# Kernel tuning notes

Measured on AMD Instinct MI355X. Metric: run time of the kernel, lower is better.

The kernel has to match this reference:

```python
import jax, jax.numpy as jnp
import numpy as np

N = 100000          # nodes (object pairs)
E = 3200000         # edges between pairs
D_IN = 12           # box-pair features
HID = 1024
OUT = 8             # 4+4 logits
C = 10              # z channels after concat (8 logits + ymin_diff + intersection)
R = 2               # relation feature dim
N_LAYERS = 3
LIT = 2 * C + R     # literals per binary clause


def setup_inputs() -> dict:
    key = jax.random.key(0)
    ks = jax.random.split(key, 10)
    features = jax.random.uniform(ks[0], (N, D_IN), dtype=jnp.float32)
    relations = jax.random.normal(ks[1], (E, R), dtype=jnp.float32)
    sx = jax.random.randint(ks[2], (E,), 0, N, dtype=jnp.int64)
    sy = jax.random.randint(ks[3], (E,), 0, N, dtype=jnp.int64)
    # MLP params (Kaiming-ish scale)
    W1 = jax.random.normal(ks[4], (D_IN, HID), dtype=jnp.float32) * (1.0 / np.sqrt(D_IN))
    b1 = jnp.zeros((HID,), dtype=jnp.float32)
    W2 = jax.random.normal(ks[5], (HID, OUT), dtype=jnp.float32) * (1.0 / np.sqrt(HID))
    b2 = jnp.zeros((OUT,), dtype=jnp.float32)
    # one clause weight per KENN relational layer
    clause_w = jax.random.normal(ks[6], (N_LAYERS,), dtype=jnp.float32) * 0.5
    return {"features": features, "relations": relations, "W1": W1, "b1": b1,
            "W2": W2, "b2": b2, "clause_w": clause_w, "sx": sx, "sy": sy}


def _kenn_layer(z, relations, sx, sy, w):
    # gather-boost-scatter: Godel boost residuum (smooth softmax approximation)
    signs = jnp.where(jnp.arange(LIT) % 2 == 0, 1.0, -1.0).astype(z.dtype)
    g = jnp.concatenate([z[sx], z[sy], relations], axis=1)      # [E, LIT]
    delta = (jax.nn.softplus(w) * jax.nn.softmax(signs * g, axis=1)) * signs
    z = z.at[sx].add(delta[:, :C])
    z = z.at[sy].add(delta[:, C:2 * C])
    return z


def reference(features, relations, W1, b1, W2, b2, clause_w, sx, sy):
    # MLP preactivations (dropout is identity at inference)
    h = jax.nn.relu(features @ W1 + b1)           # [N, 1024]
    z = h @ W2 + b2                               # [N, 8]
    ymin_diff = (features[:, 2] - features[:, -2]) * 10.0
    mask = ((features[:, 0] <= features[:, 5]) & (features[:, 1] >= features[:, 4]) &
            (features[:, 2] <= features[:, -1]) & (features[:, 3] >= features[:, -2]))
    intersection = mask.astype(z.dtype) * 10.0 - 5.0
    z = jnp.concatenate([z, ymin_diff[:, None], intersection[:, None]], axis=1)  # [N, 10]
    for l in range(N_LAYERS):
        z = _kenn_layer(z, relations, sx, sy, clause_w[l])
    z = z[:, :-2]                                 # drop the two auxiliary channels
    za, zb = z[:, :4], z[:, 4:]
    return za, jax.nn.softmax(za, axis=1), zb, jax.nn.softmax(zb, axis=1)
```

## Files before the change

kernel.cpp:

```cpp
#include <hip/hip_runtime.h>
#include <math.h>

constexpr int kN    = 100000;
constexpr int kE    = 3200000;
constexpr int kHid  = 1024;
constexpr int kZrow = 12;

constexpr int kCBShift = 10;
constexpr int kCBNodes = 1 << kCBShift;
constexpr int kCB      = (kN + kCBNodes - 1) / kCBNodes;
constexpr int kCBCap   = 68000;
constexpr int kChunkE  = 1024;
constexpr int kChunkEnt= kChunkE * 2;


__global__ __launch_bounds__(256) void mlp_kernel4(
    const float* __restrict__ feat,
    const float* __restrict__ W1,
    const float* __restrict__ b1,
    const float* __restrict__ W2,
    const float* __restrict__ b2,
    float* __restrict__ z)
{
    __shared__ float red[4][8][64];

    int wave = (int)__builtin_amdgcn_readfirstlane(threadIdx.x >> 6);
    int lane = threadIdx.x & 63;
    int n    = blockIdx.x * 64 + lane;
    bool valid = n < kN;
    int nc   = valid ? n : (kN - 1);

    const float4* fr = reinterpret_cast<const float4*>(feat + (size_t)nc * 12);
    float4 f0 = fr[0], f1 = fr[1], f2 = fr[2];
    float f[12] = {f0.x, f0.y, f0.z, f0.w,
                   f1.x, f1.y, f1.z, f1.w,
                   f2.x, f2.y, f2.z, f2.w};

    float acc[8] = {0,0,0,0,0,0,0,0};
    int k0 = wave * (kHid / 4);
    int k1 = k0 + (kHid / 4);

    #pragma unroll 4
    for (int k = k0; k < k1; ++k) {
        float h = b1[k];
        #pragma unroll
        for (int d = 0; d < 12; ++d) h = fmaf(f[d], W1[d * kHid + k], h);
        h = fmaxf(h, 0.0f);
        #pragma unroll
        for (int o = 0; o < 8; ++o) acc[o] = fmaf(h, W2[k * 8 + o], acc[o]);
    }

    #pragma unroll
    for (int o = 0; o < 8; ++o) red[wave][o][lane] = acc[o];
    __syncthreads();

    if (wave == 0 && valid) {
        float a[8];
        #pragma unroll
        for (int o = 0; o < 8; ++o)
            a[o] = red[0][o][lane] + red[1][o][lane] +
                   red[2][o][lane] + red[3][o][lane] + b2[o];

        float ymin_diff = (f[2] - f[10]) * 10.0f;
        bool mask = (f[0] <= f[5]) && (f[1] >= f[4]) &&
                    (f[2] <= f[11]) && (f[3] >= f[10]);
        float inter = mask ? 5.0f : -5.0f;

        float* zr = z + (size_t)n * kZrow;
        reinterpret_cast<float4*>(zr)[0] = {a[0], a[1], a[2], a[3]};
        reinterpret_cast<float4*>(zr)[1] = {a[4], a[5], a[6], a[7]};
        reinterpret_cast<float4*>(zr)[2] = {ymin_diff, inter, 0.0f, 0.0f};
    }
}

__global__ __launch_bounds__(256) void bucketize(
    const int* __restrict__ sx,
    const int* __restrict__ sy,
    const float* __restrict__ rel,
    int* __restrict__ gcur,
    unsigned* __restrict__ bkey,
    float2* __restrict__ brel)
{
    __shared__ int      cnt[128];
    __shared__ int      scn[128];
    __shared__ int      startArr[129];
    __shared__ int      c2[128];
    __shared__ int      gbase[128];
    __shared__ unsigned stage_k[kChunkEnt];
    __shared__ float2   stage_r[kChunkEnt];

    int tid  = threadIdx.x;
    int e0   = blockIdx.x * kChunkE;
    int ecnt = min(kChunkE, kE - e0);

    if (tid < 128) cnt[tid] = 0;
    __syncthreads();

    int ea[kChunkE / 256], eb[kChunkE / 256];
    int ne = 0;
    for (int i = tid; i < ecnt; i += 256) {
        int a = sx[e0 + i];
        int b = sy[e0 + i];
        ea[ne] = a; eb[ne] = b; ++ne;
        atomicAdd(&cnt[a >> kCBShift], 1);
        atomicAdd(&cnt[b >> kCBShift], 1);
    }
    __syncthreads();

    if (tid < 128) scn[tid] = cnt[tid];
    __syncthreads();
    for (int off = 1; off < 128; off <<= 1) {
        int v = 0;
        if (tid < 128 && tid >= off) v = scn[tid - off];
        __syncthreads();
        if (tid < 128) scn[tid] += v;
        __syncthreads();
    }
    if (tid < 128) startArr[tid] = scn[tid] - cnt[tid];
    if (tid == 127) startArr[128] = scn[127];
    __syncthreads();

    if (tid < 128) {
        int c = (tid < kCB) ? cnt[tid] : 0;
        gbase[tid] = (c > 0) ? atomicAdd(&gcur[tid], c) : 0;
        c2[tid] = startArr[tid];
    }
    __syncthreads();

    ne = 0;
    for (int i = tid; i < ecnt; i += 256) {
        int a = ea[ne], b = eb[ne]; ++ne;
        float2 r = reinterpret_cast<const float2*>(rel)[e0 + i];
        int sa = atomicAdd(&c2[a >> kCBShift], 1);
        stage_k[sa] = (unsigned)b | ((unsigned)(a & (kCBNodes - 1)) << 17);
        stage_r[sa] = r;
        int sb = atomicAdd(&c2[b >> kCBShift], 1);
        stage_k[sb] = (unsigned)a | ((unsigned)(b & (kCBNodes - 1)) << 17) | (1u << 27);
        stage_r[sb] = r;
    }
    __syncthreads();

    int total = 2 * ecnt;
    for (int j = tid; j < total; j += 256) {
        int lo = 0, hi = kCB;
        while (hi - lo > 1) {
            int mid = (lo + hi) >> 1;
            if (startArr[mid] <= j) lo = mid; else hi = mid;
        }
        int idx = gbase[lo] + (j - startArr[lo]);
        if (idx < kCBCap) {
            size_t dst = (size_t)lo * kCBCap + idx;
            bkey[dst] = stage_k[j];
            brel[dst] = stage_r[j];
        }
    }
}

__global__ __launch_bounds__(1024) void sort_bucket16(
    const int* __restrict__ gcur,
    const unsigned* __restrict__ bkey,
    const float2* __restrict__ brel,
    uint4* __restrict__ sdata,
    int* __restrict__ rowptr,
    int* __restrict__ rowcnt)
{
    __shared__ int cnt1024[kCBNodes];
    __shared__ int scanb[kCBNodes];
    __shared__ int cur[kCBNodes];

    int tid = threadIdx.x;
    int b   = blockIdx.x;
    int n   = min(gcur[b], kCBCap);
    const unsigned* bk = bkey + (size_t)b * kCBCap;
    const float2*   br = brel + (size_t)b * kCBCap;

    cnt1024[tid] = 0;
    __syncthreads();

    for (int j = tid; j < n; j += 1024)
        atomicAdd(&cnt1024[(bk[j] >> 17) & 1023u], 1);
    __syncthreads();

    scanb[tid] = cnt1024[tid];
    __syncthreads();
    for (int off = 1; off < kCBNodes; off <<= 1) {
        int v = (tid >= off) ? scanb[tid - off] : 0;
        __syncthreads();
        scanb[tid] += v;
        __syncthreads();
    }
    int excl = scanb[tid] - cnt1024[tid];
    cur[tid] = excl;

    int node = (b << kCBShift) + tid;
    if (node < kN) {
        rowptr[node] = b * kCBCap + excl;
        rowcnt[node] = cnt1024[tid];
    }
    __syncthreads();

    for (int j = tid; j < n; j += 1024) {
        unsigned k = bk[j];
        float2  r  = br[j];
        int ol = (int)((k >> 17) & 1023u);
        int pos = atomicAdd(&cur[ol], 1);
        sdata[(size_t)b * kCBCap + pos] =
            make_uint4(k, __float_as_uint(r.x), __float_as_uint(r.y), 0u);
    }
}

__global__ __launch_bounds__(256) void gather16(
    const float* __restrict__ zin,
    float* __restrict__ zout,
    const uint4* __restrict__ sdata,
    const int* __restrict__ rowptr,
    const int* __restrict__ rowcnt,
    const float* __restrict__ cw,
    int layer)
{
    int node = blockIdx.x * 16 + (threadIdx.x >> 4);
    int lane = threadIdx.x & 15;
    if (node >= kN) return;

    float w  = cw[layer];
    float sw = fmaxf(w, 0.0f) + log1pf(__expf(-fabsf(w)));

    const float* zs = zin + (size_t)node * kZrow;
    float4 s0 = reinterpret_cast<const float4*>(zs)[0];
    float4 s1 = reinterpret_cast<const float4*>(zs)[1];
    float4 s2 = reinterpret_cast<const float4*>(zs)[2];
    float self[10] = {s0.x, s0.y, s0.z, s0.w, s1.x, s1.y, s1.z, s1.w, s2.x, s2.y};

    float acc[10] = {0,0,0,0,0,0,0,0,0,0};
    int rp = rowptr[node];
    int rc = rowcnt[node];

    for (int i = lane; i < rc; i += 16) {
        uint4 ent = sdata[rp + i];
        unsigned k = ent.x;
        float rx = __uint_as_float(ent.y);
        float ry = __uint_as_float(ent.z);
        int p    = (int)(k & 0x1FFFFu);
        int side = (int)((k >> 27) & 1u);

        const float* zp = zin + (size_t)p * kZrow;
        float4 p0 = reinterpret_cast<const float4*>(zp)[0];
        float4 p1 = reinterpret_cast<const float4*>(zp)[1];
        float2 p2 = reinterpret_cast<const float2*>(zp + 8)[0];
        float part[10] = {p0.x, p0.y, p0.z, p0.w, p1.x, p1.y, p1.z, p1.w, p2.x, p2.y};

        float t[22];
        #pragma unroll
        for (int j = 0; j < 10; ++j) {
            float ga = side ? part[j] : self[j];
            float gb = side ? self[j] : part[j];
            t[j]      = (j & 1) ? -ga : ga;
            t[10 + j] = (j & 1) ? -gb : gb;
        }
        t[20] = rx;
        t[21] = -ry;

        float m = t[0];
        #pragma unroll
        for (int j = 1; j < 22; ++j) m = fmaxf(m, t[j]);

        float pe[22];
        float ssum = 0.0f;
        #pragma unroll
        for (int j = 0; j < 22; ++j) { pe[j] = __expf(t[j] - m); ssum += pe[j]; }

        float scale = sw / ssum;
        #pragma unroll
        for (int j = 0; j < 10; ++j) {
            float pv = side ? pe[10 + j] : pe[j];
            acc[j] += ((j & 1) ? -scale : scale) * pv;
        }
    }

    #pragma unroll
    for (int m16 = 8; m16 >= 1; m16 >>= 1) {
        #pragma unroll
        for (int j = 0; j < 10; ++j)
            acc[j] += __shfl_xor(acc[j], m16, 16);
    }

    if (lane == 0) {
        float* zo = zout + (size_t)node * kZrow;
        reinterpret_cast<float4*>(zo)[0] =
            {self[0] + acc[0], self[1] + acc[1], self[2] + acc[2], self[3] + acc[3]};
        reinterpret_cast<float4*>(zo)[1] =
            {self[4] + acc[4], self[5] + acc[5], self[6] + acc[6], self[7] + acc[7]};
        reinterpret_cast<float4*>(zo)[2] =
            {self[8] + acc[8], self[9] + acc[9], s2.z, s2.w};
    }
}

__global__ __launch_bounds__(256) void gather16_out(
    const float* __restrict__ zin,
    float* __restrict__ out,
    const uint4* __restrict__ sdata,
    const int* __restrict__ rowptr,
    const int* __restrict__ rowcnt,
    const float* __restrict__ cw,
    int layer)
{
    int node = blockIdx.x * 16 + (threadIdx.x >> 4);
    int lane = threadIdx.x & 15;
    if (node >= kN) return;

    float w  = cw[layer];
    float sw = fmaxf(w, 0.0f) + log1pf(__expf(-fabsf(w)));

    const float* zs = zin + (size_t)node * kZrow;
    float4 s0 = reinterpret_cast<const float4*>(zs)[0];
    float4 s1 = reinterpret_cast<const float4*>(zs)[1];
    float4 s2 = reinterpret_cast<const float4*>(zs)[2];
    float self[10] = {s0.x, s0.y, s0.z, s0.w, s1.x, s1.y, s1.z, s1.w, s2.x, s2.y};

    float acc[8] = {0,0,0,0,0,0,0,0};
    int rp = rowptr[node];
    int rc = rowcnt[node];

    for (int i = lane; i < rc; i += 16) {
        uint4 ent = sdata[rp + i];
        unsigned k = ent.x;
        float rx = __uint_as_float(ent.y);
        float ry = __uint_as_float(ent.z);
        int p    = (int)(k & 0x1FFFFu);
        int side = (int)((k >> 27) & 1u);

        const float* zp = zin + (size_t)p * kZrow;
        float4 p0 = reinterpret_cast<const float4*>(zp)[0];
        float4 p1 = reinterpret_cast<const float4*>(zp)[1];
        float2 p2 = reinterpret_cast<const float2*>(zp + 8)[0];
        float part[10] = {p0.x, p0.y, p0.z, p0.w, p1.x, p1.y, p1.z, p1.w, p2.x, p2.y};

        float t[22];
        #pragma unroll
        for (int j = 0; j < 10; ++j) {
            float ga = side ? part[j] : self[j];
            float gb = side ? self[j] : part[j];
            t[j]      = (j & 1) ? -ga : ga;
            t[10 + j] = (j & 1) ? -gb : gb;
        }
        t[20] = rx;
        t[21] = -ry;

        float m = t[0];
        #pragma unroll
        for (int j = 1; j < 22; ++j) m = fmaxf(m, t[j]);

        float pe[22];
        float ssum = 0.0f;
        #pragma unroll
        for (int j = 0; j < 22; ++j) { pe[j] = __expf(t[j] - m); ssum += pe[j]; }

        float scale = sw / ssum;
        #pragma unroll
        for (int j = 0; j < 8; ++j) {
            float pv = side ? pe[10 + j] : pe[j];
            acc[j] += ((j & 1) ? -scale : scale) * pv;
        }
    }

    #pragma unroll
    for (int m16 = 8; m16 >= 1; m16 >>= 1) {
        #pragma unroll
        for (int j = 0; j < 8; ++j)
            acc[j] += __shfl_xor(acc[j], m16, 16);
    }

    if (lane == 0) {
        float4 za = {self[0] + acc[0], self[1] + acc[1], self[2] + acc[2], self[3] + acc[3]};
        float4 zb = {self[4] + acc[4], self[5] + acc[5], self[6] + acc[6], self[7] + acc[7]};

        float ma = fmaxf(fmaxf(za.x, za.y), fmaxf(za.z, za.w));
        float ea0 = __expf(za.x - ma), ea1 = __expf(za.y - ma);
        float ea2 = __expf(za.z - ma), ea3 = __expf(za.w - ma);
        float ia = 1.0f / (ea0 + ea1 + ea2 + ea3);
        float4 sma = {ea0 * ia, ea1 * ia, ea2 * ia, ea3 * ia};

        float mb = fmaxf(fmaxf(zb.x, zb.y), fmaxf(zb.z, zb.w));
        float eb0 = __expf(zb.x - mb), eb1 = __expf(zb.y - mb);
        float eb2 = __expf(zb.z - mb), eb3 = __expf(zb.w - mb);
        float ib = 1.0f / (eb0 + eb1 + eb2 + eb3);
        float4 smb = {eb0 * ib, eb1 * ib, eb2 * ib, eb3 * ib};

        reinterpret_cast<float4*>(out)[node]           = za;
        reinterpret_cast<float4*>(out + 4 * kN)[node]  = sma;
        reinterpret_cast<float4*>(out + 8 * kN)[node]  = zb;
        reinterpret_cast<float4*>(out + 12 * kN)[node] = smb;
    }
}

__global__ __launch_bounds__(1024) void sort_bucket(
    const int* __restrict__ gcur,
    const unsigned* __restrict__ bkey,
    const float2* __restrict__ brel,
    unsigned* __restrict__ skey,
    float2* __restrict__ srel,
    int* __restrict__ rowptr,
    int* __restrict__ rowcnt)
{
    __shared__ int cnt1024[kCBNodes];
    __shared__ int scanb[kCBNodes];
    __shared__ int cur[kCBNodes];

    int tid = threadIdx.x;
    int b   = blockIdx.x;
    int n   = min(gcur[b], kCBCap);
    const unsigned* bk = bkey + (size_t)b * kCBCap;
    const float2*   br = brel + (size_t)b * kCBCap;

    cnt1024[tid] = 0;
    __syncthreads();
    for (int j = tid; j < n; j += 1024)
        atomicAdd(&cnt1024[(bk[j] >> 17) & 1023u], 1);
    __syncthreads();

    scanb[tid] = cnt1024[tid];
    __syncthreads();
    for (int off = 1; off < kCBNodes; off <<= 1) {
        int v = (tid >= off) ? scanb[tid - off] : 0;
        __syncthreads();
        scanb[tid] += v;
        __syncthreads();
    }
    int excl = scanb[tid] - cnt1024[tid];
    cur[tid] = excl;

    int node = (b << kCBShift) + tid;
    if (node < kN) {
        rowptr[node] = b * kCBCap + excl;
        rowcnt[node] = cnt1024[tid];
    }
    __syncthreads();

    for (int j = tid; j < n; j += 1024) {
        unsigned k = bk[j];
        float2  r  = br[j];
        int ol = (int)((k >> 17) & 1023u);
        int pos = atomicAdd(&cur[ol], 1);
        size_t dst = (size_t)b * kCBCap + pos;
        skey[dst] = k;
        srel[dst] = r;
    }
}

__global__ __launch_bounds__(256) void kenn_gather_csr(
    const float* __restrict__ zin,
    float* __restrict__ zout,
    const unsigned* __restrict__ skey,
    const float2* __restrict__ srel,
    const int* __restrict__ rowptr,
    const int* __restrict__ rowcnt,
    const float* __restrict__ cw,
    int layer)
{
    int node = blockIdx.x * 16 + (threadIdx.x >> 4);
    int lane = threadIdx.x & 15;
    if (node >= kN) return;

    float w  = cw[layer];
    float sw = fmaxf(w, 0.0f) + log1pf(__expf(-fabsf(w)));

    const float* zs = zin + (size_t)node * kZrow;
    float4 s0 = reinterpret_cast<const float4*>(zs)[0];
    float4 s1 = reinterpret_cast<const float4*>(zs)[1];
    float4 s2 = reinterpret_cast<const float4*>(zs)[2];
    float self[10] = {s0.x, s0.y, s0.z, s0.w, s1.x, s1.y, s1.z, s1.w, s2.x, s2.y};

    float acc[10] = {0,0,0,0,0,0,0,0,0,0};
    int rp = rowptr[node];
    int rc = rowcnt[node];

    for (int i = lane; i < rc; i += 16) {
        unsigned k = skey[rp + i];
        float2  r  = srel[rp + i];
        int p    = (int)(k & 0x1FFFFu);
        int side = (int)((k >> 27) & 1u);

        const float* zp = zin + (size_t)p * kZrow;
        float4 p0 = reinterpret_cast<const float4*>(zp)[0];
        float4 p1 = reinterpret_cast<const float4*>(zp)[1];
        float2 p2 = reinterpret_cast<const float2*>(zp + 8)[0];
        float part[10] = {p0.x, p0.y, p0.z, p0.w, p1.x, p1.y, p1.z, p1.w, p2.x, p2.y};

        float t[22];
        #pragma unroll
        for (int j = 0; j < 10; ++j) {
            float ga = side ? part[j] : self[j];
            float gb = side ? self[j] : part[j];
            t[j]      = (j & 1) ? -ga : ga;
            t[10 + j] = (j & 1) ? -gb : gb;
        }
        t[20] = r.x;
        t[21] = -r.y;

        float m = t[0];
        #pragma unroll
        for (int j = 1; j < 22; ++j) m = fmaxf(m, t[j]);

        float pe[22];
        float ssum = 0.0f;
        #pragma unroll
        for (int j = 0; j < 22; ++j) { pe[j] = __expf(t[j] - m); ssum += pe[j]; }

        float scale = sw / ssum;
        #pragma unroll
        for (int j = 0; j < 10; ++j) {
            float pv = side ? pe[10 + j] : pe[j];
            acc[j] += ((j & 1) ? -scale : scale) * pv;
        }
    }

    #pragma unroll
    for (int m16 = 8; m16 >= 1; m16 >>= 1) {
        #pragma unroll
        for (int j = 0; j < 10; ++j)
            acc[j] += __shfl_xor(acc[j], m16, 16);
    }

    if (lane == 0) {
        float* zo = zout + (size_t)node * kZrow;
        reinterpret_cast<float4*>(zo)[0] =
            {self[0] + acc[0], self[1] + acc[1], self[2] + acc[2], self[3] + acc[3]};
        reinterpret_cast<float4*>(zo)[1] =
            {self[4] + acc[4], self[5] + acc[5], self[6] + acc[6], self[7] + acc[7]};
        reinterpret_cast<float4*>(zo)[2] =
            {self[8] + acc[8], self[9] + acc[9], s2.z, s2.w};
    }
}

__global__ __launch_bounds__(256) void out_kernel(
    const float* __restrict__ z,
    float* __restrict__ out)
{
    int n = blockIdx.x * blockDim.x + threadIdx.x;
    if (n >= kN) return;

    const float* zr = z + (size_t)n * kZrow;
    float4 za = reinterpret_cast<const float4*>(zr)[0];
    float4 zb = reinterpret_cast<const float4*>(zr)[1];

    float ma = fmaxf(fmaxf(za.x, za.y), fmaxf(za.z, za.w));
    float ea0 = __expf(za.x - ma), ea1 = __expf(za.y - ma);
    float ea2 = __expf(za.z - ma), ea3 = __expf(za.w - ma);
    float ia = 1.0f / (ea0 + ea1 + ea2 + ea3);
    float4 sma = {ea0 * ia, ea1 * ia, ea2 * ia, ea3 * ia};

    float mb = fmaxf(fmaxf(zb.x, zb.y), fmaxf(zb.z, zb.w));
    float eb0 = __expf(zb.x - mb), eb1 = __expf(zb.y - mb);
    float eb2 = __expf(zb.z - mb), eb3 = __expf(zb.w - mb);
    float ib = 1.0f / (eb0 + eb1 + eb2 + eb3);
    float4 smb = {eb0 * ib, eb1 * ib, eb2 * ib, eb3 * ib};

    reinterpret_cast<float4*>(out)[n]           = za;
    reinterpret_cast<float4*>(out + 4 * kN)[n]  = sma;
    reinterpret_cast<float4*>(out + 8 * kN)[n]  = zb;
    reinterpret_cast<float4*>(out + 12 * kN)[n] = smb;
}

__global__ __launch_bounds__(256) void edge_kernel(
    const float* __restrict__ zin,
    float* __restrict__ zout,
    const float* __restrict__ rel,
    const int* __restrict__ sx,
    const int* __restrict__ sy,
    const float* __restrict__ cw,
    int layer)
{
    int e = blockIdx.x * blockDim.x + threadIdx.x;
    if (e >= kE) return;

    float w  = cw[layer];
    float sw = fmaxf(w, 0.0f) + log1pf(__expf(-fabsf(w)));

    int a = sx[e];
    int b = sy[e];
    float2 r = reinterpret_cast<const float2*>(rel)[e];

    const float* za = zin + (size_t)a * kZrow;
    const float* zb = zin + (size_t)b * kZrow;
    float4 a0 = reinterpret_cast<const float4*>(za)[0];
    float4 a1 = reinterpret_cast<const float4*>(za)[1];
    float2 a2 = reinterpret_cast<const float2*>(za + 8)[0];
    float4 b0 = reinterpret_cast<const float4*>(zb)[0];
    float4 b1v = reinterpret_cast<const float4*>(zb)[1];
    float2 b2v = reinterpret_cast<const float2*>(zb + 8)[0];

    float t[22];
    t[0]  =  a0.x;  t[1]  = -a0.y;  t[2]  =  a0.z;  t[3]  = -a0.w;
    t[4]  =  a1.x;  t[5]  = -a1.y;  t[6]  =  a1.z;  t[7]  = -a1.w;
    t[8]  =  a2.x;  t[9]  = -a2.y;
    t[10] =  b0.x;  t[11] = -b0.y;  t[12] =  b0.z;  t[13] = -b0.w;
    t[14] =  b1v.x; t[15] = -b1v.y; t[16] =  b1v.z; t[17] = -b1v.w;
    t[18] =  b2v.x; t[19] = -b2v.y;
    t[20] =  r.x;   t[21] = -r.y;

    float m = t[0];
    #pragma unroll
    for (int i = 1; i < 22; ++i) m = fmaxf(m, t[i]);
    float p[22]; float s = 0.0f;
    #pragma unroll
    for (int i = 0; i < 22; ++i) { p[i] = __expf(t[i] - m); s += p[i]; }
    float scale = sw / s;

    float* oa = zout + (size_t)a * kZrow;
    float* ob = zout + (size_t)b * kZrow;
    #pragma unroll
    for (int i = 0; i < 10; ++i)
        unsafeAtomicAdd(oa + i, ((i & 1) ? -scale : scale) * p[i]);
    #pragma unroll
    for (int i = 0; i < 10; ++i)
        unsafeAtomicAdd(ob + i, ((i & 1) ? -scale : scale) * p[10 + i]);
}

extern "C" void kernel_launch(void* const* d_in, const int* in_sizes, int n_in,
                              void* d_out, int out_size, void* d_ws, size_t ws_size,
                              hipStream_t stream)
{
    const float* feat = (const float*)d_in[0];
    const float* rel  = (const float*)d_in[1];
    const float* W1   = (const float*)d_in[2];
    const float* b1   = (const float*)d_in[3];
    const float* W2   = (const float*)d_in[4];
    const float* b2   = (const float*)d_in[5];
    const float* cw   = (const float*)d_in[6];
    const int*   sx   = (const int*)d_in[7];
    const int*   sy   = (const int*)d_in[8];
    float* out = (float*)d_out;

    char* ws = (char*)d_ws;
    const size_t off_zA     = 0;
    const size_t off_zB     = 4800000;
    const size_t off_gcur   = 9600000;
    const size_t off_rowptr = 9600512;
    const size_t off_rowcnt = 10000896;
    const size_t off_bkey   = 10401280;
    const size_t off_brel   = 37057280;
    const size_t off_sdata  = 90369280;
    const size_t need_t1    = 196993280;
    const size_t off_skey   = off_sdata;
    const size_t off_srel   = 117025280;
    const size_t need_t2    = 170337280;

    float*    zA     = (float*)(ws + off_zA);
    float*    zB     = (float*)(ws + off_zB);
    int*      gcur   = (int*)(ws + off_gcur);
    int*      rowptr = (int*)(ws + off_rowptr);
    int*      rowcnt = (int*)(ws + off_rowcnt);
    unsigned* bkey   = (unsigned*)(ws + off_bkey);
    float2*   brel   = (float2*)(ws + off_brel);
    uint4*    sdata  = (uint4*)(ws + off_sdata);
    unsigned* skey   = (unsigned*)(ws + off_skey);
    float2*   srel   = (float2*)(ws + off_srel);

    dim3 blk(256);
    dim3 gN((kN + 255) / 256);
    dim3 gE((kE + 255) / 256);
    dim3 gB((kE + kChunkE - 1) / kChunkE);
    dim3 gG(kN / 16);
    dim3 gM((kN + 63) / 64);

    mlp_kernel4<<<gM, blk, 0, stream>>>(feat, W1, b1, W2, b2, zA);

    if (ws_size >= need_t1) {
        hipMemsetAsync(gcur, 0, 512, stream);
        bucketize<<<gB, blk, 0, stream>>>(sx, sy, rel, gcur, bkey, brel);
        sort_bucket16<<<dim3(kCB), dim3(1024), 0, stream>>>(gcur, bkey, brel,
                                                            sdata, rowptr, rowcnt);
        gather16<<<gG, blk, 0, stream>>>(zA, zB, sdata, rowptr, rowcnt, cw, 0);
        gather16<<<gG, blk, 0, stream>>>(zB, zA, sdata, rowptr, rowcnt, cw, 1);
        gather16_out<<<gG, blk, 0, stream>>>(zA, out, sdata, rowptr, rowcnt, cw, 2);
    } else if (ws_size >= need_t2) {
        hipMemsetAsync(gcur, 0, 512, stream);
        bucketize<<<gB, blk, 0, stream>>>(sx, sy, rel, gcur, bkey, brel);
        sort_bucket<<<dim3(kCB), dim3(1024), 0, stream>>>(gcur, bkey, brel,
                                                          skey, srel, rowptr, rowcnt);
        kenn_gather_csr<<<gG, blk, 0, stream>>>(zA, zB, skey, srel, rowptr, rowcnt, cw, 0);
        kenn_gather_csr<<<gG, blk, 0, stream>>>(zB, zA, skey, srel, rowptr, rowcnt, cw, 1);
        kenn_gather_csr<<<gG, blk, 0, stream>>>(zA, zB, skey, srel, rowptr, rowcnt, cw, 2);
        out_kernel<<<gN, blk, 0, stream>>>(zB, out);
    } else {
        size_t zbytes = (size_t)kN * kZrow * sizeof(float);
        hipMemcpyAsync(zB, zA, zbytes, hipMemcpyDeviceToDevice, stream);
        edge_kernel<<<gE, blk, 0, stream>>>(zA, zB, rel, sx, sy, cw, 0);
        hipMemcpyAsync(zA, zB, zbytes, hipMemcpyDeviceToDevice, stream);
        edge_kernel<<<gE, blk, 0, stream>>>(zB, zA, rel, sx, sy, cw, 1);
        hipMemcpyAsync(zB, zA, zbytes, hipMemcpyDeviceToDevice, stream);
        edge_kernel<<<gE, blk, 0, stream>>>(zA, zB, rel, sx, sy, cw, 2);
        out_kernel<<<gN, blk, 0, stream>>>(zB, out);
    }
}
```

Before: 591.0 us.

## Split per-bucket counting sort into segmented histogram, scan, and scatter kernels

Replaces the single sort_bucket16 kernel, which launched only about 98 blocks (one per bucket), with three kernels. Each bucket is split into 8 segments that compute local histograms, a per-bucket scan turns them into per-segment base offsets, and 8 blocks per bucket scatter into the sorted layout. This raises parallelism across the GPU's compute units for the sort stage. In exchange it adds two kernel launches and an extra global histogram buffer, and it slightly shrinks the bucket capacity.

```diff
diff --git a/kernel.cpp b/kernel.cpp
--- a/kernel.cpp
+++ b/kernel.cpp
@@ -9,7 +9,8 @@
 constexpr int kCBShift = 10;
 constexpr int kCBNodes = 1 << kCBShift;
 constexpr int kCB      = (kN + kCBNodes - 1) / kCBNodes;
-constexpr int kCBCap   = 68000;
+constexpr int kCBCap   = 66800;
+constexpr int kSeg     = 8;
 constexpr int kChunkE  = 1024;
 constexpr int kChunkEnt= kChunkE * 2;
 
@@ -156,32 +157,50 @@
     }
 }
 
-__global__ __launch_bounds__(1024) void sort_bucket16(
+__global__ __launch_bounds__(1024) void seg_hist(
     const int* __restrict__ gcur,
     const unsigned* __restrict__ bkey,
-    const float2* __restrict__ brel,
-    uint4* __restrict__ sdata,
+    int* __restrict__ seghist)
+{
+    __shared__ int hist[kCBNodes];
+
+    int tid = threadIdx.x;
+    int b   = blockIdx.x / kSeg;
+    int s   = blockIdx.x % kSeg;
+    int n   = min(gcur[b], kCBCap);
+    int j0  = (int)((long long)n * s / kSeg);
+    int j1  = (int)((long long)n * (s + 1) / kSeg);
+    const unsigned* bk = bkey + (size_t)b * kCBCap;
+
+    hist[tid] = 0;
+    __syncthreads();
+
+    for (int j = j0 + tid; j < j1; j += 1024)
+        atomicAdd(&hist[(bk[j] >> 17) & 1023u], 1);
+    __syncthreads();
+
+    seghist[(size_t)blockIdx.x * kCBNodes + tid] = hist[tid];
+}
+
+__global__ __launch_bounds__(1024) void seg_base(
+    int* __restrict__ seghist,
     int* __restrict__ rowptr,
     int* __restrict__ rowcnt)
 {
-    __shared__ int cnt1024[kCBNodes];
     __shared__ int scanb[kCBNodes];
-    __shared__ int cur[kCBNodes];
 
     int tid = threadIdx.x;
     int b   = blockIdx.x;
-    int n   = min(gcur[b], kCBCap);
-    const unsigned* bk = bkey + (size_t)b * kCBCap;
-    const float2*   br = brel + (size_t)b * kCBCap;
-
-    cnt1024[tid] = 0;
-    __syncthreads();
-
-    for (int j = tid; j < n; j += 1024)
-        atomicAdd(&cnt1024[(bk[j] >> 17) & 1023u], 1);
-    __syncthreads();
-
-    scanb[tid] = cnt1024[tid];
+
+    int c[kSeg];
+    int tot = 0;
+    #pragma unroll
+    for (int s = 0; s < kSeg; ++s) {
+        c[s] = seghist[((size_t)(b * kSeg + s)) * kCBNodes + tid];
+        tot += c[s];
+    }
+
+    scanb[tid] = tot;
     __syncthreads();
     for (int off = 1; off < kCBNodes; off <<= 1) {
         int v = (tid >= off) ? scanb[tid - off] : 0;
@@ -189,17 +208,44 @@
         scanb[tid] += v;
         __syncthreads();
     }
-    int excl = scanb[tid] - cnt1024[tid];
-    cur[tid] = excl;
+    int excl = scanb[tid] - tot;
 
     int node = (b << kCBShift) + tid;
     if (node < kN) {
         rowptr[node] = b * kCBCap + excl;
-        rowcnt[node] = cnt1024[tid];
-    }
-    __syncthreads();
-
-    for (int j = tid; j < n; j += 1024) {
+        rowcnt[node] = tot;
+    }
+
+    int base = excl;
+    #pragma unroll
+    for (int s = 0; s < kSeg; ++s) {
+        seghist[((size_t)(b * kSeg + s)) * kCBNodes + tid] = base;
+        base += c[s];
+    }
+}
+
+__global__ __launch_bounds__(1024) void seg_scatter(
+    const int* __restrict__ gcur,
+    const unsigned* __restrict__ bkey,
+    const float2* __restrict__ brel,
+    const int* __restrict__ seghist,
+    uint4* __restrict__ sdata)
+{
+    __shared__ int cur[kCBNodes];
+
+    int tid = threadIdx.x;
+    int b   = blockIdx.x / kSeg;
+    int s   = blockIdx.x % kSeg;
+    int n   = min(gcur[b], kCBCap);
+    int j0  = (int)((long long)n * s / kSeg);
+    int j1  = (int)((long long)n * (s + 1) / kSeg);
+    const unsigned* bk = bkey + (size_t)b * kCBCap;
+    const float2*   br = brel + (size_t)b * kCBCap;
+
+    cur[tid] = seghist[(size_t)blockIdx.x * kCBNodes + tid];
+    __syncthreads();
+
+    for (int j = j0 + tid; j < j1; j += 1024) {
         unsigned k = bk[j];
         float2  r  = br[j];
         int ol = (int)((k >> 17) & 1023u);
@@ -632,29 +678,31 @@
     float* out = (float*)d_out;
 
     char* ws = (char*)d_ws;
-    const size_t off_zA     = 0;
-    const size_t off_zB     = 4800000;
-    const size_t off_gcur   = 9600000;
-    const size_t off_rowptr = 9600512;
-    const size_t off_rowcnt = 10000896;
-    const size_t off_bkey   = 10401280;
-    const size_t off_brel   = 37057280;
-    const size_t off_sdata  = 90369280;
-    const size_t need_t1    = 196993280;
-    const size_t off_skey   = off_sdata;
-    const size_t off_srel   = 117025280;
-    const size_t need_t2    = 170337280;
-
-    float*    zA     = (float*)(ws + off_zA);
-    float*    zB     = (float*)(ws + off_zB);
-    int*      gcur   = (int*)(ws + off_gcur);
-    int*      rowptr = (int*)(ws + off_rowptr);
-    int*      rowcnt = (int*)(ws + off_rowcnt);
-    unsigned* bkey   = (unsigned*)(ws + off_bkey);
-    float2*   brel   = (float2*)(ws + off_brel);
-    uint4*    sdata  = (uint4*)(ws + off_sdata);
-    unsigned* skey   = (unsigned*)(ws + off_skey);
-    float2*   srel   = (float2*)(ws + off_srel);
+    const size_t off_zA      = 0;
+    const size_t off_zB      = 4800000;
+    const size_t off_gcur    = 9600000;
+    const size_t off_rowptr  = 9600512;
+    const size_t off_rowcnt  = 10000896;
+    const size_t off_seghist = 10401280;
+    const size_t off_bkey    = 13612544;
+    const size_t off_brel    = 39798144;
+    const size_t off_sdata   = 92169344;
+    const size_t need_t1     = 196911744;
+    const size_t off_skey    = off_sdata;
+    const size_t off_srel    = 118354944;
+    const size_t need_t2     = 170726144;
+
+    float*    zA      = (float*)(ws + off_zA);
+    float*    zB      = (float*)(ws + off_zB);
+    int*      gcur    = (int*)(ws + off_gcur);
+    int*      rowptr  = (int*)(ws + off_rowptr);
+    int*      rowcnt  = (int*)(ws + off_rowcnt);
+    int*      seghist = (int*)(ws + off_seghist);
+    unsigned* bkey    = (unsigned*)(ws + off_bkey);
+    float2*   brel    = (float2*)(ws + off_brel);
+    uint4*    sdata   = (uint4*)(ws + off_sdata);
+    unsigned* skey    = (unsigned*)(ws + off_skey);
+    float2*   srel    = (float2*)(ws + off_srel);
 
     dim3 blk(256);
     dim3 gN((kN + 255) / 256);
@@ -662,14 +710,16 @@
     dim3 gB((kE + kChunkE - 1) / kChunkE);
     dim3 gG(kN / 16);
     dim3 gM((kN + 63) / 64);
+    dim3 gS(kCB * kSeg);
 
     mlp_kernel4<<<gM, blk, 0, stream>>>(feat, W1, b1, W2, b2, zA);
 
     if (ws_size >= need_t1) {
         hipMemsetAsync(gcur, 0, 512, stream);
         bucketize<<<gB, blk, 0, stream>>>(sx, sy, rel, gcur, bkey, brel);
-        sort_bucket16<<<dim3(kCB), dim3(1024), 0, stream>>>(gcur, bkey, brel,
-                                                            sdata, rowptr, rowcnt);
+        seg_hist   <<<gS, dim3(1024), 0, stream>>>(gcur, bkey, seghist);
+        seg_base   <<<dim3(kCB), dim3(1024), 0, stream>>>(seghist, rowptr, rowcnt);
+        seg_scatter<<<gS, dim3(1024), 0, stream>>>(gcur, bkey, brel, seghist, sdata);
         gather16<<<gG, blk, 0, stream>>>(zA, zB, sdata, rowptr, rowcnt, cw, 0);
         gather16<<<gG, blk, 0, stream>>>(zB, zA, sdata, rowptr, rowcnt, cw, 1);
         gather16_out<<<gG, blk, 0, stream>>>(zA, out, sdata, rowptr, rowcnt, cw, 2);
```

Measured after the change: 559.6 us. 1.06x faster.
